# Optimization experiments

Hardware: AMD Instinct MI355X
Metric: run time of the kernel (lower is better)

## Reference

```python
import jax, jax.numpy as jnp
import numpy as np

B, T, C = 2, 2048, 2048
NH, NKV, HD = 16, 8, 256
SOFTCAP = 50.0
ROPE_BASE = 10000.0


def setup_inputs() -> dict:
    key = jax.random.key(0)
    ks = jax.random.split(key, 5)
    s = 0.02
    return {
        "X": jax.random.normal(ks[0], (B, T, C), dtype=jnp.float32),
        "Wq": jax.random.normal(ks[1], (C, NH * HD), dtype=jnp.float32) * s,
        "Wk": jax.random.normal(ks[2], (C, NKV * HD), dtype=jnp.float32) * s,
        "Wv": jax.random.normal(ks[3], (C, NKV * HD), dtype=jnp.float32) * s,
        "Wo": jax.random.normal(ks[4], (NH * HD, C), dtype=jnp.float32) * s,
    }


def _rotate_half(x):
    x1, x2 = x[..., : x.shape[-1] // 2], x[..., x.shape[-1] // 2 :]
    return jnp.concatenate((-x2, x1), axis=-1)


def _rope_cos_sin(t, head_dim, dtype):
    inv_freq = 1.0 / ROPE_BASE ** (
        jnp.arange(0, head_dim, 2, dtype=jnp.int32).astype(jnp.float32) / head_dim
    )  # [HD/2]
    pos = jnp.arange(t, dtype=jnp.float32)  # [T]
    freqs = pos[:, None] * inv_freq[None, :]  # [T, HD/2]
    emb = jnp.concatenate((freqs, freqs), axis=-1)  # [T, HD]
    # shape [1, 1, T, HD] to broadcast over (B, H, T, HD)
    return (
        jnp.cos(emb).astype(dtype)[None, None],
        jnp.sin(emb).astype(dtype)[None, None],
    )


def reference(X, Wq, Wk, Wv, Wo):
    b, t, c = X.shape
    n_rep = NH // NKV

    q = (X @ Wq).reshape(b, t, NH, HD).transpose(0, 2, 1, 3)   # [B,NH,T,HD]
    k = (X @ Wk).reshape(b, t, NKV, HD).transpose(0, 2, 1, 3)  # [B,NKV,T,HD]
    v = (X @ Wv).reshape(b, t, NKV, HD).transpose(0, 2, 1, 3)

    cos, sin = _rope_cos_sin(t, HD, X.dtype)
    q = q * cos + _rotate_half(q) * sin
    k = k * cos + _rotate_half(k) * sin

    # repeat_kv (GQA): [B,NKV,T,HD] -> [B,NH,T,HD]
    k = jnp.repeat(k, n_rep, axis=1)
    v = jnp.repeat(v, n_rep, axis=1)

    scale = 256.0 ** (-0.5)  # hardcoded in source
    att = jnp.einsum("bhqd,bhkd->bhqk", q, k) * scale
    # tanh logit softcapping
    att = SOFTCAP * jnp.tanh(att / SOFTCAP)
    # causal mask
    causal = jnp.tril(jnp.ones((t, t), dtype=bool))
    att = jnp.where(causal[None, None], att, -jnp.inf)
    att = jax.nn.softmax(att, axis=-1)

    y = jnp.einsum("bhqk,bhkd->bhqd", att, v)  # [B,NH,T,HD]
    y = y.transpose(0, 2, 1, 3).reshape(b, t, NH * HD)
    return y @ Wo
```

## Files before the change

kernel.cpp:

```cpp
#include <hip/hip_runtime.h>
#include <hip/hip_bf16.h>

#define NHD 16
#define NKVH 8
#define HDIM 256
#define TSEQ 2048
#define BATCH 2

typedef unsigned int   u32;
typedef unsigned short u16;

typedef __attribute__((ext_vector_type(8))) short bf16x8;
typedef __attribute__((ext_vector_type(4))) float floatx4;

__device__ inline u32 cvt2bf(float lo, float hi) {
  u32 r;
  asm("v_cvt_pk_bf16_f32 %0, %1, %2" : "=v"(r) : "v"(lo), "v"(hi));
  return r;
}
__device__ inline u16 f2bf(float f) {
  union { float f; u32 i; } v; v.f = f;
  u32 r = v.i + 0x7fffu + ((v.i >> 16) & 1u);
  return (u16)(r >> 16);
}
__device__ inline float bf2f(u16 u) {
  union { u32 i; float f; } v; v.i = ((u32)u) << 16; return v.f;
}

typedef const __attribute__((address_space(1))) u32* gptr_t;
typedef __attribute__((address_space(3))) u32* lptr_t;
__device__ inline void gl_lds16(const void* g, void* l) {
  __builtin_amdgcn_global_load_lds((gptr_t)g, (lptr_t)l, 16, 0, 0);
}

__global__ __launch_bounds__(256) void tconv_k(
    const float* __restrict__ in, u16* __restrict__ out, int R, int Cc)
{
  __shared__ float tile[64][65];
  const int r0 = blockIdx.y * 64, c0 = blockIdx.x * 64;
  const int tr = threadIdx.x >> 4;
  const int tc = (threadIdx.x & 15) * 4;
#pragma unroll
  for (int j = 0; j < 4; ++j) {
    float4 v = *(const float4*)(in + (size_t)(r0 + tr + j * 16) * Cc + c0 + tc);
    tile[tr + j * 16][tc + 0] = v.x;
    tile[tr + j * 16][tc + 1] = v.y;
    tile[tr + j * 16][tc + 2] = v.z;
    tile[tr + j * 16][tc + 3] = v.w;
  }
  __syncthreads();
#pragma unroll
  for (int j = 0; j < 4; ++j) {
    int c = tr + j * 16;
    u16 o[4];
#pragma unroll
    for (int i = 0; i < 4; ++i) o[i] = f2bf(tile[tc + i][c]);
    *(uint2*)(out + (size_t)(c0 + c) * R + r0 + tc) = *(const uint2*)o;
  }
}

__global__ __launch_bounds__(256) void xconv_k(
    const float* __restrict__ in, u16* __restrict__ out)
{
  size_t i = (size_t)blockIdx.x * 256 + threadIdx.x;
  float4 a = *(const float4*)(in + i * 8);
  float4 b = *(const float4*)(in + i * 8 + 4);
  uint4 o;
  o.x = cvt2bf(a.x, a.y); o.y = cvt2bf(a.z, a.w);
  o.z = cvt2bf(b.x, b.y); o.w = cvt2bf(b.z, b.w);
  *(uint4*)(out + i * 8) = o;
}

template<int EPI>
__global__ __launch_bounds__(512, 2) void gemm256_k(
    const u16* __restrict__ Ab, const u16* __restrict__ BTp,
    void* __restrict__ Op, int M, int N, int K)
{
  __shared__ u16 LA[2][256 * 64];
  __shared__ u16 LB[2][256 * 64];
  const int t = threadIdx.x;
  const int lane = t & 63, wave = t >> 6;
  const int lg = lane >> 4, l15 = lane & 15;
  const int wm = wave >> 2, wn = wave & 3;
  const int mtiles = M >> 8;
  const int mt = (int)blockIdx.x % mtiles, nt = (int)blockIdx.x / mtiles;
  const int m0 = mt << 8, n0 = nt << 8;

  const int srow = wave * 32 + (lane >> 3);
  const int sk   = ((lane & 7) ^ (srow & 7)) << 3;
  const u16* Ag = Ab  + (size_t)(m0 + srow) * K + sk;
  const u16* Bg = BTp + (size_t)(n0 + srow) * K + sk;

  auto STAGE = [&](int k0, int sel) {
#pragma unroll
    for (int q = 0; q < 4; ++q)
      gl_lds16(Ag + k0 + (size_t)q * 8 * K, &LA[sel][(wave * 32 + q * 8) * 64]);
#pragma unroll
    for (int q = 0; q < 4; ++q)
      gl_lds16(Bg + k0 + (size_t)q * 8 * K, &LB[sel][(wave * 32 + q * 8) * 64]);
  };

  floatx4 acc[8][4];
#pragma unroll
  for (int i = 0; i < 8; ++i)
#pragma unroll
    for (int j = 0; j < 4; ++j) acc[i][j] = (floatx4){0.f, 0.f, 0.f, 0.f};

  STAGE(0, 0);
  const int KT = K >> 6;
  for (int kt = 0; kt < KT; ++kt) {
    const int sel = kt & 1;
    if (kt + 1 < KT) {
      STAGE((kt + 1) << 6, sel ^ 1);
      asm volatile("s_waitcnt vmcnt(8)" ::: "memory");
    } else {
      asm volatile("s_waitcnt vmcnt(0)" ::: "memory");
    }
    __builtin_amdgcn_s_barrier();
    __builtin_amdgcn_sched_barrier(0);
#pragma unroll
    for (int ks = 0; ks < 2; ++ks) {
      const int c = (ks << 2) + lg;
      bf16x8 bfv[4];
#pragma unroll
      for (int j = 0; j < 4; ++j) {
        int row = wn * 64 + (j << 4) + l15;
        bfv[j] = *(const bf16x8*)(&LB[sel][row * 64 + ((c ^ (row & 7)) << 3)]);
      }
#pragma unroll
      for (int i = 0; i < 8; ++i) {
        int row = wm * 128 + (i << 4) + l15;
        bf16x8 af = *(const bf16x8*)(&LA[sel][row * 64 + ((c ^ (row & 7)) << 3)]);
#pragma unroll
        for (int j = 0; j < 4; ++j)
          acc[i][j] = __builtin_amdgcn_mfma_f32_16x16x32_bf16(af, bfv[j], acc[i][j], 0, 0, 0);
      }
    }
    __builtin_amdgcn_s_barrier();
  }

#pragma unroll
  for (int i = 0; i < 8; ++i) {
#pragma unroll
    for (int j = 0; j < 4; ++j) {
#pragma unroll
      for (int r = 0; r < 4; ++r) {
        int m = m0 + wm * 128 + (i << 4) + (lg << 2) + r;
        int n = n0 + wn * 64 + (j << 4) + l15;
        float v = acc[i][j][r];
        int bb = m >> 11, tt = m & 2047;
        if (EPI == 0) {
          ((float*)Op)[(size_t)m * N + n] = v;
        } else if (EPI == 1) {
          int h = n >> 8, d = n & 255;
          ((u16*)Op)[(((size_t)bb * NHD + h) * TSEQ + tt) * HDIM + d] = f2bf(v);
        } else {
          if (n < 2048) {
            int h = n >> 8, d = n & 255;
            ((u16*)Op)[(((size_t)bb * NKVH + h) * TSEQ + tt) * HDIM + d] = f2bf(v);
          } else {
            int n2 = n - 2048;
            int h = n2 >> 8, d = n2 & 255;
            ((u16*)Op)[8388608u + (((size_t)bb * NKVH + h) * HDIM + d) * TSEQ + tt] = f2bf(v);
          }
        }
      }
    }
  }
}

__global__ __launch_bounds__(256) void rope_k(u16* buf) {
  size_t idx = (size_t)blockIdx.x * 256 + threadIdx.x;
  int d = (int)(idx & 127);
  size_t rest = idx >> 7;
  int tt = (int)(rest & (TSEQ - 1));
  float invf = exp2f(-(float)d * 0.103810253f);
  float th = (float)tt * invf;
  float sn, cs;
  sincosf(th, &sn, &cs);
  size_t base = rest * HDIM;
  float x1 = bf2f(buf[base + d]);
  float x2 = bf2f(buf[base + d + 128]);
  buf[base + d]       = f2bf(x1 * cs - x2 * sn);
  buf[base + d + 128] = f2bf(x2 * cs + x1 * sn);
}

__global__ __launch_bounds__(512, 2) void attn_k(
    const u16* __restrict__ Q, const u16* __restrict__ Kb,
    const u16* __restrict__ Vt, u16* __restrict__ Y)
{
  __shared__ u16 Ks2[2][64 * 256];
  __shared__ u16 Vs2[2][256 * 64];
  __shared__ u16 Ps[8 * 16 * 64];
  __shared__ float Ls[8][16];
  const int t = threadIdx.x, lane = t & 63, w = t >> 6;
  const int lg = lane >> 4, l15 = lane & 15;
  const int qt = 15 - (int)blockIdx.y;
  const int h = (int)blockIdx.x >> 1, b = (int)blockIdx.x & 1;
  const int hkv = h >> 1;

  const u16* Kg = Kb + ((size_t)(b * NKVH + hkv)) * TSEQ * HDIM;
  const u16* Vg = Vt + ((size_t)(b * NKVH + hkv)) * HDIM * TSEQ;

  int koff[4], voff[4];
#pragma unroll
  for (int q = 0; q < 4; ++q) {
    int g = w * 4 + q;
    int krow = g * 2 + (lane >> 5);
    int kcc = lane & 31;
    koff[q] = krow * 256 + ((kcc ^ (krow & 7)) << 3);
    int vd = g * 8 + (lane >> 3);
    int vcc = lane & 7;
    voff[q] = vd * 2048 + ((vcc ^ (vd & 7)) << 3);
  }

  auto STAGE = [&](int st, int sel) {
    const u16* kbase = Kg + (size_t)st * (64 * 256);
    const u16* vbase = Vg + st * 64;
#pragma unroll
    for (int q = 0; q < 4; ++q)
      gl_lds16(kbase + koff[q], &Ks2[sel][(w * 4 + q) * 512]);
#pragma unroll
    for (int q = 0; q < 4; ++q)
      gl_lds16(vbase + voff[q], &Vs2[sel][(w * 4 + q) * 512]);
  };

  const u16* Qg = Q + (((size_t)(b * NHD + h)) * TSEQ + qt * 128 + w * 16 + l15) * HDIM;
  bf16x8 qf[8];
#pragma unroll
  for (int ks = 0; ks < 8; ++ks) qf[ks] = *(const bf16x8*)(Qg + ks * 32 + lg * 8);

  floatx4 accY[16];
#pragma unroll
  for (int i = 0; i < 16; ++i) accY[i] = (floatx4){0.f, 0.f, 0.f, 0.f};
  float rsum = 0.f;

  const int qglob = qt * 128 + w * 16 + l15;
  const int qmax  = qt * 128 + w * 16 + 15;
  const int nst = 2 * qt + 2;

  STAGE(0, 0);
  for (int st = 0; st < nst; ++st) {
    const int sel = st & 1;
    if (st + 1 < nst) {
      STAGE(st + 1, sel ^ 1);
      asm volatile("s_waitcnt vmcnt(8)" ::: "memory");
    } else {
      asm volatile("s_waitcnt vmcnt(0)" ::: "memory");
    }
    __builtin_amdgcn_s_barrier();
    __builtin_amdgcn_sched_barrier(0);

    if (st * 64 <= qmax) {
#pragma unroll
      for (int stile = 0; stile < 4; ++stile) {
        floatx4 sa = (floatx4){0.f, 0.f, 0.f, 0.f};
#pragma unroll
        for (int ks = 0; ks < 8; ++ks) {
          int row = (stile << 4) + l15;
          int c = (ks << 2) + lg;
          bf16x8 kf = *(const bf16x8*)((const char*)Ks2[sel] +
                        row * 512 + (((c ^ (row & 7)) & 31) << 4));
          sa = __builtin_amdgcn_mfma_f32_16x16x32_bf16(kf, qf[ks], sa, 0, 0, 0);
        }
        int sbase = st * 64 + (stile << 4) + (lg << 2);
        float p[4];
#pragma unroll
        for (int r = 0; r < 4; ++r) {
          float z = sa[r] * 0.0625f;
          float u = __expf(z * 0.04f);
          float pv = __expf(-100.0f / (u + 1.0f));
          pv = (sbase + r <= qglob) ? pv : 0.0f;
          p[r] = pv;
          rsum += pv;
        }
        uint2 pw;
        pw.x = cvt2bf(p[0], p[1]);
        pw.y = cvt2bf(p[2], p[3]);
        int o = (stile << 5) + (lg << 3);
        int chunk = o >> 4;
        *(uint2*)((char*)Ps + (w << 11) + l15 * 128 + ((chunk ^ (l15 & 7)) << 4) + (o & 15)) = pw;
      }
#pragma unroll
      for (int ss = 0; ss < 2; ++ss) {
        int c = (ss << 2) + lg;
        bf16x8 pf = *(const bf16x8*)((const char*)Ps + (w << 11) + l15 * 128 +
                      ((c ^ (l15 & 7)) << 4));
#pragma unroll
        for (int dt = 0; dt < 16; ++dt) {
          int row = (dt << 4) + l15;
          bf16x8 vf = *(const bf16x8*)((const char*)Vs2[sel] +
                        row * 128 + (((c ^ (row & 7)) & 7) << 4));
          accY[dt] = __builtin_amdgcn_mfma_f32_16x16x32_bf16(pf, vf, accY[dt], 0, 0, 0);
        }
      }
    }
    __builtin_amdgcn_s_barrier();
  }

  rsum += __shfl_xor(rsum, 16);
  rsum += __shfl_xor(rsum, 32);
  if (lane < 16) Ls[w][l15] = rsum;
  __syncthreads();
  float inv[4];
#pragma unroll
  for (int r = 0; r < 4; ++r) inv[r] = 1.0f / Ls[w][(lg << 2) + r];

  u16* Yg = Y + ((size_t)(b * TSEQ + qt * 128 + w * 16)) * (NHD * HDIM) + h * HDIM;
#pragma unroll
  for (int dt = 0; dt < 16; ++dt)
#pragma unroll
    for (int r = 0; r < 4; ++r)
      Yg[(size_t)((lg << 2) + r) * (NHD * HDIM) + (dt << 4) + l15] =
          f2bf(accY[dt][r] * inv[r]);
}

extern "C" void kernel_launch(void* const* d_in, const int* in_sizes, int n_in,
                              void* d_out, int out_size, void* d_ws, size_t ws_size,
                              hipStream_t stream) {
  const float* X  = (const float*)d_in[0];
  const float* Wq = (const float*)d_in[1];
  const float* Wk = (const float*)d_in[2];
  const float* Wv = (const float*)d_in[3];
  const float* Wo = (const float*)d_in[4];
  float* out = (float*)d_out;

  u16* ws   = (u16*)d_ws;
  u16* XB   = ws;
  u16* WT   = ws + 8388608;
  u16* Qb   = ws + 16777216;
  u16* KVb  = ws + 33554432;
  u16* Yb   = ws;
  u16* WoT  = ws + 16777216;

  dim3 blk(256);
  xconv_k<<<dim3(4096), blk, 0, stream>>>(X, XB);
  tconv_k<<<dim3(64, 32), blk, 0, stream>>>(Wq, WT, 2048, 4096);
  gemm256_k<1><<<dim3(16 * 16), dim3(512), 0, stream>>>(XB, WT, Qb, 4096, 4096, 2048);
  tconv_k<<<dim3(32, 32), blk, 0, stream>>>(Wk, WT, 2048, 2048);
  tconv_k<<<dim3(32, 32), blk, 0, stream>>>(Wv, WT + (size_t)2048 * 2048, 2048, 2048);
  gemm256_k<3><<<dim3(16 * 16), dim3(512), 0, stream>>>(XB, WT, KVb, 4096, 4096, 2048);
  rope_k<<<dim3((BATCH * NHD  * TSEQ * 128) / 256), blk, 0, stream>>>(Qb);
  rope_k<<<dim3((BATCH * NKVH * TSEQ * 128) / 256), blk, 0, stream>>>(KVb);
  attn_k<<<dim3(32, 16), dim3(512), 0, stream>>>(Qb, KVb, KVb + 8388608, Yb);
  tconv_k<<<dim3(32, 64), blk, 0, stream>>>(Wo, WoT, 4096, 2048);
  gemm256_k<0><<<dim3(16 * 8), dim3(512), 0, stream>>>(Yb, WoT, out, 4096, 2048, 4096);
}
```

Measured before the change: 458.5 us.

## Shrink attention tiles, add BM=128 output GEMM, raw exp/rcp, setprio

Attention blocks drop from 512 to 256 threads with 64-query and 32-key tiles, and the grid grows to 32x32. This gives more blocks and finer causal granularity, with the P and V LDS swizzles redone to match. The output projection GEMM gets a templated BM=128 variant so it launches 256 blocks instead of 128 and fills more CUs. The softcap exp is rewritten with raw v_exp_f32/v_rcp_f32, and s_setprio wraps the MFMA sections. Smaller attention tiles mean less reuse per K/V load and more load traffic overall.

Result: faster. 424.9 us (-7.3%).

```diff
diff --git a/kernel.cpp b/kernel.cpp
--- a/kernel.cpp
+++ b/kernel.cpp
@@ -25,6 +25,12 @@
 }
 __device__ inline float bf2f(u16 u) {
   union { u32 i; float f; } v; v.i = ((u32)u) << 16; return v.f;
+}
+__device__ inline float fexp2(float x) {
+  float r; asm("v_exp_f32 %0, %1" : "=v"(r) : "v"(x)); return r;
+}
+__device__ inline float frcp(float x) {
+  float r; asm("v_rcp_f32 %0, %1" : "=v"(r) : "v"(x)); return r;
 }
 
 typedef const __attribute__((address_space(1))) u32* gptr_t;
@@ -71,38 +77,42 @@
   *(uint4*)(out + i * 8) = o;
 }
 
-template<int EPI>
+template<int EPI, int BM>
 __global__ __launch_bounds__(512, 2) void gemm256_k(
     const u16* __restrict__ Ab, const u16* __restrict__ BTp,
     void* __restrict__ Op, int M, int N, int K)
 {
-  __shared__ u16 LA[2][256 * 64];
+  constexpr int NI = BM / 32;
+  constexpr int AI = BM / 64;
+  __shared__ u16 LA[2][BM * 64];
   __shared__ u16 LB[2][256 * 64];
   const int t = threadIdx.x;
   const int lane = t & 63, wave = t >> 6;
   const int lg = lane >> 4, l15 = lane & 15;
   const int wm = wave >> 2, wn = wave & 3;
-  const int mtiles = M >> 8;
+  const int mtiles = M / BM;
   const int mt = (int)blockIdx.x % mtiles, nt = (int)blockIdx.x / mtiles;
-  const int m0 = mt << 8, n0 = nt << 8;
-
-  const int srow = wave * 32 + (lane >> 3);
-  const int sk   = ((lane & 7) ^ (srow & 7)) << 3;
-  const u16* Ag = Ab  + (size_t)(m0 + srow) * K + sk;
-  const u16* Bg = BTp + (size_t)(n0 + srow) * K + sk;
+  const int m0 = mt * BM, n0 = nt << 8;
+
+  const int arow = wave * (BM / 8) + (lane >> 3);
+  const int ska  = ((lane & 7) ^ (arow & 7)) << 3;
+  const int brow = wave * 32 + (lane >> 3);
+  const int skb  = ((lane & 7) ^ (brow & 7)) << 3;
+  const u16* Ag = Ab  + (size_t)(m0 + arow) * K + ska;
+  const u16* Bg = BTp + (size_t)(n0 + brow) * K + skb;
 
   auto STAGE = [&](int k0, int sel) {
 #pragma unroll
-    for (int q = 0; q < 4; ++q)
-      gl_lds16(Ag + k0 + (size_t)q * 8 * K, &LA[sel][(wave * 32 + q * 8) * 64]);
+    for (int q = 0; q < AI; ++q)
+      gl_lds16(Ag + k0 + (size_t)q * 8 * K, &LA[sel][(wave * (BM / 8) + q * 8) * 64]);
 #pragma unroll
     for (int q = 0; q < 4; ++q)
       gl_lds16(Bg + k0 + (size_t)q * 8 * K, &LB[sel][(wave * 32 + q * 8) * 64]);
   };
 
-  floatx4 acc[8][4];
-#pragma unroll
-  for (int i = 0; i < 8; ++i)
+  floatx4 acc[NI][4];
+#pragma unroll
+  for (int i = 0; i < NI; ++i)
 #pragma unroll
     for (int j = 0; j < 4; ++j) acc[i][j] = (floatx4){0.f, 0.f, 0.f, 0.f};
 
@@ -112,12 +122,14 @@
     const int sel = kt & 1;
     if (kt + 1 < KT) {
       STAGE((kt + 1) << 6, sel ^ 1);
-      asm volatile("s_waitcnt vmcnt(8)" ::: "memory");
+      if constexpr (BM == 256) asm volatile("s_waitcnt vmcnt(8)" ::: "memory");
+      else                     asm volatile("s_waitcnt vmcnt(6)" ::: "memory");
     } else {
       asm volatile("s_waitcnt vmcnt(0)" ::: "memory");
     }
     __builtin_amdgcn_s_barrier();
     __builtin_amdgcn_sched_barrier(0);
+    __builtin_amdgcn_s_setprio(1);
 #pragma unroll
     for (int ks = 0; ks < 2; ++ks) {
       const int c = (ks << 2) + lg;
@@ -128,24 +140,25 @@
         bfv[j] = *(const bf16x8*)(&LB[sel][row * 64 + ((c ^ (row & 7)) << 3)]);
       }
 #pragma unroll
-      for (int i = 0; i < 8; ++i) {
-        int row = wm * 128 + (i << 4) + l15;
+      for (int i = 0; i < NI; ++i) {
+        int row = wm * (BM / 2) + (i << 4) + l15;
         bf16x8 af = *(const bf16x8*)(&LA[sel][row * 64 + ((c ^ (row & 7)) << 3)]);
 #pragma unroll
         for (int j = 0; j < 4; ++j)
           acc[i][j] = __builtin_amdgcn_mfma_f32_16x16x32_bf16(af, bfv[j], acc[i][j], 0, 0, 0);
       }
     }
+    __builtin_amdgcn_s_setprio(0);
     __builtin_amdgcn_s_barrier();
   }
 
 #pragma unroll
-  for (int i = 0; i < 8; ++i) {
+  for (int i = 0; i < NI; ++i) {
 #pragma unroll
     for (int j = 0; j < 4; ++j) {
 #pragma unroll
       for (int r = 0; r < 4; ++r) {
-        int m = m0 + wm * 128 + (i << 4) + (lg << 2) + r;
+        int m = m0 + wm * (BM / 2) + (i << 4) + (lg << 2) + r;
         int n = n0 + wn * 64 + (j << 4) + l15;
         float v = acc[i][j][r];
         int bb = m >> 11, tt = m & 2047;
@@ -185,17 +198,17 @@
   buf[base + d + 128] = f2bf(x2 * cs + x1 * sn);
 }
 
-__global__ __launch_bounds__(512, 2) void attn_k(
+__global__ __launch_bounds__(256, 2) void attn_k(
     const u16* __restrict__ Q, const u16* __restrict__ Kb,
     const u16* __restrict__ Vt, u16* __restrict__ Y)
 {
-  __shared__ u16 Ks2[2][64 * 256];
-  __shared__ u16 Vs2[2][256 * 64];
-  __shared__ u16 Ps[8 * 16 * 64];
-  __shared__ float Ls[8][16];
+  __shared__ u16 Ks2[2][32 * 256];
+  __shared__ u16 Vs2[2][256 * 32];
+  __shared__ u16 Ps[4 * 16 * 32];
+  __shared__ float Ls[4][16];
   const int t = threadIdx.x, lane = t & 63, w = t >> 6;
   const int lg = lane >> 4, l15 = lane & 15;
-  const int qt = 15 - (int)blockIdx.y;
+  const int qt = 31 - (int)blockIdx.y;
   const int h = (int)blockIdx.x >> 1, b = (int)blockIdx.x & 1;
   const int hkv = h >> 1;
 
@@ -205,27 +218,25 @@
   int koff[4], voff[4];
 #pragma unroll
   for (int q = 0; q < 4; ++q) {
-    int g = w * 4 + q;
-    int krow = g * 2 + (lane >> 5);
-    int kcc = lane & 31;
+    int krow = w * 8 + q * 2 + (lane >> 5);
+    int kcc  = lane & 31;
     koff[q] = krow * 256 + ((kcc ^ (krow & 7)) << 3);
-    int vd = g * 8 + (lane >> 3);
-    int vcc = lane & 7;
-    voff[q] = vd * 2048 + ((vcc ^ (vd & 7)) << 3);
+    int vd  = w * 64 + q * 16 + (lane >> 2);
+    voff[q] = vd * TSEQ + (((lane & 3) ^ ((vd >> 2) & 3)) << 3);
   }
 
   auto STAGE = [&](int st, int sel) {
-    const u16* kbase = Kg + (size_t)st * (64 * 256);
-    const u16* vbase = Vg + st * 64;
+    const u16* kbase = Kg + (size_t)st * (32 * 256);
+    const u16* vbase = Vg + st * 32;
 #pragma unroll
     for (int q = 0; q < 4; ++q)
-      gl_lds16(kbase + koff[q], &Ks2[sel][(w * 4 + q) * 512]);
+      gl_lds16(kbase + koff[q], &Ks2[sel][(w * 8 + q * 2) * 256]);
 #pragma unroll
     for (int q = 0; q < 4; ++q)
-      gl_lds16(vbase + voff[q], &Vs2[sel][(w * 4 + q) * 512]);
+      gl_lds16(vbase + voff[q], &Vs2[sel][(w * 64 + q * 16) * 32]);
   };
 
-  const u16* Qg = Q + (((size_t)(b * NHD + h)) * TSEQ + qt * 128 + w * 16 + l15) * HDIM;
+  const u16* Qg = Q + (((size_t)(b * NHD + h)) * TSEQ + qt * 64 + w * 16 + l15) * HDIM;
   bf16x8 qf[8];
 #pragma unroll
   for (int ks = 0; ks < 8; ++ks) qf[ks] = *(const bf16x8*)(Qg + ks * 32 + lg * 8);
@@ -235,9 +246,10 @@
   for (int i = 0; i < 16; ++i) accY[i] = (floatx4){0.f, 0.f, 0.f, 0.f};
   float rsum = 0.f;
 
-  const int qglob = qt * 128 + w * 16 + l15;
-  const int qmax  = qt * 128 + w * 16 + 15;
+  const int qglob = qt * 64 + w * 16 + l15;
+  const int qmaxw = qt * 64 + w * 16 + 15;
   const int nst = 2 * qt + 2;
+  const int fps = (l15 ^ (l15 >> 2)) & 3;
 
   STAGE(0, 0);
   for (int st = 0; st < nst; ++st) {
@@ -251,25 +263,25 @@
     __builtin_amdgcn_s_barrier();
     __builtin_amdgcn_sched_barrier(0);
 
-    if (st * 64 <= qmax) {
-#pragma unroll
-      for (int stile = 0; stile < 4; ++stile) {
+    if (st * 32 <= qmaxw) {
+      __builtin_amdgcn_s_setprio(1);
+#pragma unroll
+      for (int stile = 0; stile < 2; ++stile) {
         floatx4 sa = (floatx4){0.f, 0.f, 0.f, 0.f};
 #pragma unroll
         for (int ks = 0; ks < 8; ++ks) {
           int row = (stile << 4) + l15;
           int c = (ks << 2) + lg;
           bf16x8 kf = *(const bf16x8*)((const char*)Ks2[sel] +
-                        row * 512 + (((c ^ (row & 7)) & 31) << 4));
+                        row * 512 + ((c ^ (row & 7)) << 4));
           sa = __builtin_amdgcn_mfma_f32_16x16x32_bf16(kf, qf[ks], sa, 0, 0, 0);
         }
-        int sbase = st * 64 + (stile << 4) + (lg << 2);
+        int sbase = st * 32 + (stile << 4) + (lg << 2);
         float p[4];
 #pragma unroll
         for (int r = 0; r < 4; ++r) {
-          float z = sa[r] * 0.0625f;
-          float u = __expf(z * 0.04f);
-          float pv = __expf(-100.0f / (u + 1.0f));
+          float u = fexp2(sa[r] * 0.0036067376f);
+          float pv = fexp2(-144.26950408f * frcp(u + 1.0f));
           pv = (sbase + r <= qglob) ? pv : 0.0f;
           p[r] = pv;
           rsum += pv;
@@ -278,22 +290,21 @@
         pw.x = cvt2bf(p[0], p[1]);
         pw.y = cvt2bf(p[2], p[3]);
         int o = (stile << 5) + (lg << 3);
-        int chunk = o >> 4;
-        *(uint2*)((char*)Ps + (w << 11) + l15 * 128 + ((chunk ^ (l15 & 7)) << 4) + (o & 15)) = pw;
-      }
-#pragma unroll
-      for (int ss = 0; ss < 2; ++ss) {
-        int c = (ss << 2) + lg;
-        bf16x8 pf = *(const bf16x8*)((const char*)Ps + (w << 11) + l15 * 128 +
-                      ((c ^ (l15 & 7)) << 4));
+        int gran = (o >> 4) ^ fps;
+        *(uint2*)((char*)Ps + (w << 10) + l15 * 64 + (gran << 4) + (o & 15)) = pw;
+      }
+      {
+        bf16x8 pf = *(const bf16x8*)((const char*)Ps + (w << 10) + l15 * 64 +
+                      ((lg ^ fps) << 4));
 #pragma unroll
         for (int dt = 0; dt < 16; ++dt) {
           int row = (dt << 4) + l15;
           bf16x8 vf = *(const bf16x8*)((const char*)Vs2[sel] +
-                        row * 128 + (((c ^ (row & 7)) & 7) << 4));
+                        row * 64 + ((lg ^ ((row >> 2) & 3)) << 4));
           accY[dt] = __builtin_amdgcn_mfma_f32_16x16x32_bf16(pf, vf, accY[dt], 0, 0, 0);
         }
       }
+      __builtin_amdgcn_s_setprio(0);
     }
     __builtin_amdgcn_s_barrier();
   }
@@ -306,7 +317,7 @@
 #pragma unroll
   for (int r = 0; r < 4; ++r) inv[r] = 1.0f / Ls[w][(lg << 2) + r];
 
-  u16* Yg = Y + ((size_t)(b * TSEQ + qt * 128 + w * 16)) * (NHD * HDIM) + h * HDIM;
+  u16* Yg = Y + ((size_t)(b * TSEQ + qt * 64 + w * 16)) * (NHD * HDIM) + h * HDIM;
 #pragma unroll
   for (int dt = 0; dt < 16; ++dt)
 #pragma unroll
@@ -336,13 +347,13 @@
   dim3 blk(256);
   xconv_k<<<dim3(4096), blk, 0, stream>>>(X, XB);
   tconv_k<<<dim3(64, 32), blk, 0, stream>>>(Wq, WT, 2048, 4096);
-  gemm256_k<1><<<dim3(16 * 16), dim3(512), 0, stream>>>(XB, WT, Qb, 4096, 4096, 2048);
+  gemm256_k<1, 256><<<dim3(16 * 16), dim3(512), 0, stream>>>(XB, WT, Qb, 4096, 4096, 2048);
   tconv_k<<<dim3(32, 32), blk, 0, stream>>>(Wk, WT, 2048, 2048);
   tconv_k<<<dim3(32, 32), blk, 0, stream>>>(Wv, WT + (size_t)2048 * 2048, 2048, 2048);
-  gemm256_k<3><<<dim3(16 * 16), dim3(512), 0, stream>>>(XB, WT, KVb, 4096, 4096, 2048);
+  gemm256_k<3, 256><<<dim3(16 * 16), dim3(512), 0, stream>>>(XB, WT, KVb, 4096, 4096, 2048);
   rope_k<<<dim3((BATCH * NHD  * TSEQ * 128) / 256), blk, 0, stream>>>(Qb);
   rope_k<<<dim3((BATCH * NKVH * TSEQ * 128) / 256), blk, 0, stream>>>(KVb);
-  attn_k<<<dim3(32, 16), dim3(512), 0, stream>>>(Qb, KVb, KVb + 8388608, Yb);
+  attn_k<<<dim3(32, 32), blk, 0, stream>>>(Qb, KVb, KVb + 8388608, Yb);
   tconv_k<<<dim3(32, 64), blk, 0, stream>>>(Wo, WoT, 4096, 2048);
-  gemm256_k<0><<<dim3(16 * 8), dim3(512), 0, stream>>>(Yb, WoT, out, 4096, 2048, 4096);
-}
+  gemm256_k<0, 128><<<dim3(32 * 8), dim3(512), 0, stream>>>(Yb, WoT, out, 4096, 2048, 4096);
+}
```
